# Performance work log

Hardware: AMD Instinct MI355X
Metric: run time of the kernel (lower is better)

Reference implementation:

```python
import jax, jax.numpy as jnp
import numpy as np

N_USERS = 100000
N_ITEMS = 50000
N_NODES = N_USERS + N_ITEMS
N_EDGES = 4800000
EMB_DIM = 64
N_LAYERS = 3


def setup_inputs() -> dict:
    key = jax.random.key(0)
    k1, k2, k3, k4, k5 = jax.random.split(key, 5)
    user_emb = jax.random.normal(k1, (N_USERS, EMB_DIM), dtype=jnp.float32)
    item_emb = jax.random.normal(k2, (N_ITEMS, EMB_DIM), dtype=jnp.float32)
    # COO representation of the (symmetric-normalized) adjacency matrix
    edge_src = jax.random.randint(k3, (N_EDGES,), 0, N_NODES, dtype=jnp.int32)
    edge_dst = jax.random.randint(k4, (N_EDGES,), 0, N_NODES, dtype=jnp.int32)
    edge_weight = jax.random.uniform(k5, (N_EDGES,), dtype=jnp.float32)
    return {
        "user_emb": user_emb,
        "item_emb": item_emb,
        "edge_weight": edge_weight,
        "edge_src": edge_src,
        "edge_dst": edge_dst,
    }


def _spmm(edge_src, edge_dst, edge_weight, x):
    # out[i] = sum_j A[i, j] * x[j]  with A in COO (dst=row i, src=col j)
    msgs = edge_weight[:, None] * x[edge_src]  # [E, D]
    return jax.ops.segment_sum(msgs, edge_dst, num_segments=N_NODES)


def reference(user_emb, item_emb, edge_weight, edge_src, edge_dst):
    ego = jnp.concatenate([user_emb, item_emb], axis=0)  # [N, D]
    acc = ego  # running sum over layer embeddings (layer 0 included)
    for _ in range(N_LAYERS):
        ego = _spmm(edge_src, edge_dst, edge_weight, ego)
        acc = acc + ego
    mean_emb = acc / jnp.float32(N_LAYERS + 1)  # mean over (L+1) layers
    new_user = mean_emb[:N_USERS]
    new_item = mean_emb[N_USERS:]
    return new_user, new_item
```

## Files before the change

### kernel.cpp

```cpp
#include <hip/hip_runtime.h>
#include <hip/hip_fp16.h>

#define N_USERS 100000
#define N_ITEMS 50000
#define N_NODES 150000
#define N_EDGES 4800000
#define EMB 64
#define N_LAYERS 3

#define NBKT 256
#define NPB  586
#define NREP 8
#define SUBCAP 2624
#define CAP (NREP * SUBCAP)

typedef unsigned int u32;
typedef unsigned short u16;
typedef u32 vu4 __attribute__((ext_vector_type(4)));
typedef u32 vu2 __attribute__((ext_vector_type(2)));
typedef float vf4 __attribute__((ext_vector_type(4)));

#define W_BITS 14
#define W_SCALE 16384.0f
#define W_INV   (1.0f / 16384.0f)
#define W_MASK  16383u

__device__ __forceinline__ float2 h2f(u32 v) {
    float2 r;
    r.x = __half2float(__ushort_as_half((u16)(v & 0xffffu)));
    r.y = __half2float(__ushort_as_half((u16)(v >> 16)));
    return r;
}

__global__ void k_init(const float4* __restrict__ user,
                       const float4* __restrict__ item,
                       ushort4* __restrict__ cur,
                       int* __restrict__ cursor) {
    int i = blockIdx.x * blockDim.x + threadIdx.x;
    const int total4 = N_NODES * EMB / 4;
    const int user4  = N_USERS * EMB / 4;
    if (i < NREP * NBKT) cursor[i] = 0;
    if (i >= total4) return;
    float4 v = (i < user4) ? user[i] : item[i - user4];
    ushort4 h;
    h.x = __half_as_ushort(__float2half_rn(v.x));
    h.y = __half_as_ushort(__float2half_rn(v.y));
    h.z = __half_as_ushort(__float2half_rn(v.z));
    h.w = __half_as_ushort(__float2half_rn(v.w));
    cur[i] = h;
}

__global__ __launch_bounds__(256) void k_p1(const int4*   __restrict__ src4,
                                            const int4*   __restrict__ dst4,
                                            const float4* __restrict__ w4,
                                            int* __restrict__ cursor,
                                            u32* __restrict__ pk_arr,
                                            u16* __restrict__ ld_arr) {
    __shared__ int hist[NBKT];
    __shared__ int base[NBKT];
    int tid = threadIdx.x;
    hist[tid] = 0;
    __syncthreads();

    int g0 = blockIdx.x * 512 + tid * 2;
    bool act = (g0 < N_EDGES / 4);

    u32 pk[8];
    u32 meta[8];
    if (act) {
        int4 d0 = dst4[g0], d1 = dst4[g0 + 1];
        int4 s0 = src4[g0], s1 = src4[g0 + 1];
        float4 f0 = w4[g0], f1 = w4[g0 + 1];
        int   ds[8] = {d0.x, d0.y, d0.z, d0.w, d1.x, d1.y, d1.z, d1.w};
        int   ss[8] = {s0.x, s0.y, s0.z, s0.w, s1.x, s1.y, s1.z, s1.w};
        float wf[8] = {f0.x, f0.y, f0.z, f0.w, f1.x, f1.y, f1.z, f1.w};
        #pragma unroll
        for (int k = 0; k < 8; ++k) {
            u32 d  = (u32)ds[k];
            u32 b  = d / NPB;
            u32 ld = d - b * NPB;
            int r  = atomicAdd(&hist[b], 1);
            u32 wq = (u32)(wf[k] * W_SCALE + 0.5f);
            if (wq > W_MASK) wq = W_MASK;
            pk[k]   = ((u32)ss[k] << W_BITS) | wq;
            meta[k] = ((u32)r << 18) | (b << 10) | ld;
        }
    }
    __syncthreads();

    int rep = blockIdx.x & (NREP - 1);
    int h = hist[tid];
    if (h > 0) base[tid] = atomicAdd(&cursor[rep * NBKT + tid], h);
    __syncthreads();

    if (act) {
        #pragma unroll
        for (int k = 0; k < 8; ++k) {
            u32 b  = (meta[k] >> 10) & 255u;
            u32 r  = meta[k] >> 18;
            u32 ld = meta[k] & 1023u;
            int pos = base[b] + (int)r;
            if (pos < SUBCAP) {
                size_t slot = (size_t)b * CAP + (size_t)rep * SUBCAP + pos;
                pk_arr[slot] = pk[k];
                ld_arr[slot] = (u16)ld;
            }
        }
    }
}

__global__ __launch_bounds__(1024) void k_p2(const int* __restrict__ cursor,
                                             const u32* __restrict__ pk_arr,
                                             const u16* __restrict__ ld_arr,
                                             int* __restrict__ row_ptr,
                                             u32* __restrict__ pairs) {
    __shared__ int hist[1024];
    __shared__ int cur[NPB];
    __shared__ int btot[NBKT];
    __shared__ int bsum[NBKT];
    int b = blockIdx.x;
    int tid = threadIdx.x;
    hist[tid] = 0;
    if (tid < NBKT) {
        int s = 0;
        #pragma unroll
        for (int r = 0; r < NREP; ++r) s += cursor[r * NBKT + tid];
        btot[tid] = s;
        bsum[tid] = s;
    }
    if (b == 0 && tid == 0) row_ptr[N_NODES] = N_EDGES;
    __syncthreads();
    for (int off = 1; off < NBKT; off <<= 1) {
        int t = 0;
        if (tid < NBKT && tid >= off) t = bsum[tid - off];
        __syncthreads();
        if (tid < NBKT && tid >= off) bsum[tid] += t;
        __syncthreads();
    }
    int gbase = bsum[b] - btot[b];

    int lo = b * NPB;
    int nb = N_NODES - lo; if (nb > NPB) nb = NPB;

    int n[NREP];
    #pragma unroll
    for (int r = 0; r < NREP; ++r) {
        int c = cursor[r * NBKT + b];
        n[r] = (c > SUBCAP) ? SUBCAP : c;
    }

    for (int r = 0; r < NREP; ++r) {
        const u16* p = ld_arr + (size_t)b * CAP + (size_t)r * SUBCAP;
        for (int i = tid; i < n[r]; i += 1024)
            atomicAdd(&hist[p[i]], 1);
    }
    __syncthreads();

    int val = hist[tid];
    for (int off = 1; off < 1024; off <<= 1) {
        int t = 0;
        if (tid >= off) t = hist[tid - off];
        __syncthreads();
        if (tid >= off) hist[tid] += t;
        __syncthreads();
    }
    int excl = hist[tid] - val;
    if (tid < nb) {
        row_ptr[lo + tid] = gbase + excl;
        cur[tid] = excl;
    }
    __syncthreads();

    for (int r = 0; r < NREP; ++r) {
        const u16* p = ld_arr + (size_t)b * CAP + (size_t)r * SUBCAP;
        const u32* q = pk_arr + (size_t)b * CAP + (size_t)r * SUBCAP;
        for (int i = tid; i < n[r]; i += 1024) {
            int ld  = p[i];
            int pos = atomicAdd(&cur[ld], 1);
            pairs[gbase + pos] = q[i];
        }
    }
}

struct Dec4 { u32 r0, r1, r2, r3; float w0, w1, w2, w3; };

__device__ __forceinline__ Dec4 dec_fast(vu4 p) {
    Dec4 d;
    d.r0 = p.x >> W_BITS; d.w0 = (float)(p.x & W_MASK) * W_INV;
    d.r1 = p.y >> W_BITS; d.w1 = (float)(p.y & W_MASK) * W_INV;
    d.r2 = p.z >> W_BITS; d.w2 = (float)(p.z & W_MASK) * W_INV;
    d.r3 = p.w >> W_BITS; d.w3 = (float)(p.w & W_MASK) * W_INV;
    return d;
}

__device__ __forceinline__ Dec4 dec_mask(vu4 p, int eb, int beg, int end) {
    Dec4 d;
    bool v0 = (eb + 0 >= beg) && (eb + 0 < end);
    bool v1 = (eb + 1 >= beg) && (eb + 1 < end);
    bool v2 = (eb + 2 >= beg) && (eb + 2 < end);
    bool v3 = (eb + 3 >= beg) && (eb + 3 < end);
    d.r0 = v0 ? (p.x >> W_BITS) : 0u; d.w0 = v0 ? (float)(p.x & W_MASK) * W_INV : 0.f;
    d.r1 = v1 ? (p.y >> W_BITS) : 0u; d.w1 = v1 ? (float)(p.y & W_MASK) * W_INV : 0.f;
    d.r2 = v2 ? (p.z >> W_BITS) : 0u; d.w2 = v2 ? (float)(p.z & W_MASK) * W_INV : 0.f;
    d.r3 = v3 ? (p.w >> W_BITS) : 0u; d.w3 = v3 ? (float)(p.w & W_MASK) * W_INV : 0.f;
    return d;
}

__device__ __forceinline__ Dec4 dec(vu4 p, int lo, int beg, int end, int g) {
    if (lo >= beg && lo + 16 <= end) return dec_fast(p);
    return dec_mask(p, lo + 4 * g, beg, end);
}

__device__ __forceinline__ vu2 ldx(const char* xbase, u32 r, u32 moff) {
    return *(const vu2*)(xbase + (size_t)(r * 128u + moff));
}

__device__ __forceinline__ void fmix2(float& a0, float& a1, float w, u32 x) {
    asm("v_fma_mix_f32 %0, %1, %2, %0 op_sel:[0,0,0] op_sel_hi:[0,1,0]"
        : "+v"(a0) : "v"(w), "v"(x));
    asm("v_fma_mix_f32 %0, %1, %2, %0 op_sel:[0,1,0] op_sel_hi:[0,1,0]"
        : "+v"(a1) : "v"(w), "v"(x));
}

__device__ __forceinline__ void acc4(vu2 xv, float w,
                                     float& ax, float& ay, float& az, float& aw) {
    fmix2(ax, ay, w, xv.x);
    fmix2(az, aw, w, xv.y);
}

#define LOADX(pfx, d) \
    vu2 pfx##0 = ldx(xbase, d.r0, moff), pfx##1 = ldx(xbase, d.r1, moff), \
        pfx##2 = ldx(xbase, d.r2, moff), pfx##3 = ldx(xbase, d.r3, moff)
#define ACCX(pfx, d) \
    acc4(pfx##0, d.w0, ax, ay, az, aw); acc4(pfx##1, d.w1, ax, ay, az, aw); \
    acc4(pfx##2, d.w2, ax, ay, az, aw); acc4(pfx##3, d.w3, ax, ay, az, aw)

template<int FIN>
__global__ __launch_bounds__(256) void k_gather(const int* __restrict__ row_ptr,
                                                const u32* __restrict__ pairs,
                                                const __half* __restrict__ x,
                                                __half* __restrict__ nxt,
                                                const float4* __restrict__ user,
                                                const float4* __restrict__ item,
                                                const ushort4* __restrict__ e1,
                                                const ushort4* __restrict__ e2,
                                                float* __restrict__ outp) {
    int wave = (blockIdx.x * blockDim.x + threadIdx.x) >> 6;
    int lane = threadIdx.x & 63;
    if (wave >= N_NODES) return;

    const int m = lane & 15;
    float4 ego = {};
    ushort4 pa = {}, pb = {};
    if (FIN && lane < 16) {
        size_t idx = (size_t)wave * 16 + m;
        const size_t user4 = (size_t)N_USERS * 16;
        ego = (idx < user4) ? user[idx] : item[idx - user4];
        pa = e1[idx];
        pb = e2[idx];
    }

    int beg = row_ptr[wave];
    int end = row_ptr[wave + 1];

    const int g = lane >> 4;
    const u32 moff = (u32)m << 3;
    const char* xbase = (const char*)x;

    float ax = 0.f, ay = 0.f, az = 0.f, aw = 0.f;

    int jb = beg & ~3;
    int nb = (end - jb + 15) >> 4;
    const u32* pp = pairs + jb + 4 * g;

    if (nb == 1) {
        vu4 P0 = __builtin_nontemporal_load((const vu4*)pp);
        Dec4 d0 = dec(P0, jb, beg, end, g);
        LOADX(xa, d0);
        ACCX(xa, d0);
    } else if (nb == 2) {
        vu4 P0 = __builtin_nontemporal_load((const vu4*)pp);
        vu4 P1 = __builtin_nontemporal_load((const vu4*)(pp + 16));
        Dec4 d0 = dec(P0, jb, beg, end, g);
        LOADX(xa, d0);
        Dec4 d1 = dec(P1, jb + 16, beg, end, g);
        LOADX(xc, d1);
        ACCX(xa, d0);
        ACCX(xc, d1);
    } else if (nb == 3) {
        vu4 P0 = __builtin_nontemporal_load((const vu4*)pp);
        vu4 P1 = __builtin_nontemporal_load((const vu4*)(pp + 16));
        vu4 P2 = __builtin_nontemporal_load((const vu4*)(pp + 32));
        Dec4 d0 = dec(P0, jb, beg, end, g);
        LOADX(xa, d0);
        Dec4 d1 = dec(P1, jb + 16, beg, end, g);
        LOADX(xc, d1);
        ACCX(xa, d0);
        Dec4 d2 = dec(P2, jb + 32, beg, end, g);
        LOADX(xd, d2);
        ACCX(xc, d1);
        ACCX(xd, d2);
    } else if (nb >= 4) {
        vu4 P0 = __builtin_nontemporal_load((const vu4*)pp);
        vu4 P1 = __builtin_nontemporal_load((const vu4*)(pp + 16));
        vu4 P2 = __builtin_nontemporal_load((const vu4*)(pp + 32));
        Dec4 d0 = dec(P0, jb, beg, end, g);
        LOADX(xa, d0);
        Dec4 d1 = dec(P1, jb + 16, beg, end, g);
        LOADX(xc, d1);
        ACCX(xa, d0);
        vu4 P3 = __builtin_nontemporal_load((const vu4*)(pp + 48));
        Dec4 d2 = dec(P2, jb + 32, beg, end, g);
        LOADX(xd, d2);
        ACCX(xc, d1);
        Dec4 d3 = dec(P3, jb + 48, beg, end, g);
        LOADX(xe, d3);
        ACCX(xd, d2);
        ACCX(xe, d3);
        for (int b = 4; b < nb; ++b) {
            vu4 Pl = __builtin_nontemporal_load((const vu4*)(pp + (size_t)16 * b));
            Dec4 dl = dec(Pl, jb + 16 * b, beg, end, g);
            LOADX(xf, dl);
            ACCX(xf, dl);
        }
    }

    ax += __shfl_xor(ax, 16); ax += __shfl_xor(ax, 32);
    ay += __shfl_xor(ay, 16); ay += __shfl_xor(ay, 32);
    az += __shfl_xor(az, 16); az += __shfl_xor(az, 32);
    aw += __shfl_xor(aw, 16); aw += __shfl_xor(aw, 32);

    if (lane < 16) {
        if (FIN) {
            vf4 o;
            o.x = (ego.x + __half2float(__ushort_as_half(pa.x))
                         + __half2float(__ushort_as_half(pb.x)) + ax) * 0.25f;
            o.y = (ego.y + __half2float(__ushort_as_half(pa.y))
                         + __half2float(__ushort_as_half(pb.y)) + ay) * 0.25f;
            o.z = (ego.z + __half2float(__ushort_as_half(pa.z))
                         + __half2float(__ushort_as_half(pb.z)) + az) * 0.25f;
            o.w = (ego.w + __half2float(__ushort_as_half(pa.w))
                         + __half2float(__ushort_as_half(pb.w)) + aw) * 0.25f;
            __builtin_nontemporal_store(o, (vf4*)outp + (size_t)wave * 16 + m);
        } else {
            ushort4 h;
            h.x = __half_as_ushort(__float2half_rn(ax));
            h.y = __half_as_ushort(__float2half_rn(ay));
            h.z = __half_as_ushort(__float2half_rn(az));
            h.w = __half_as_ushort(__float2half_rn(aw));
            ((ushort4*)nxt)[(size_t)wave * 16 + m] = h;
        }
    }
}

__global__ void k_spmm(const int*   __restrict__ src,
                       const int*   __restrict__ dst,
                       const float* __restrict__ w,
                       const float* __restrict__ x,
                       float*       __restrict__ y) {
    long long t = (long long)blockIdx.x * blockDim.x + threadIdx.x;
    int e = (int)(t >> 4);
    if (e >= N_EDGES) return;
    int q = (int)(t & 15);
    int   s  = src[e];
    int   d  = dst[e];
    float we = w[e];
    const float4* xs = (const float4*)(x + (long long)s * EMB);
    float4 v = xs[q];
    float* yd = y + (long long)d * EMB + q * 4;
    atomicAdd(yd + 0, we * v.x);
    atomicAdd(yd + 1, we * v.y);
    atomicAdd(yd + 2, we * v.z);
    atomicAdd(yd + 3, we * v.w);
}

__global__ void k_init_f32(const float4* __restrict__ user,
                           const float4* __restrict__ item,
                           float4* __restrict__ out,
                           float4* __restrict__ cur) {
    int i = blockIdx.x * blockDim.x + threadIdx.x;
    const int total4 = N_NODES * EMB / 4;
    const int user4  = N_USERS * EMB / 4;
    if (i >= total4) return;
    float4 v = (i < user4) ? user[i] : item[i - user4];
    out[i] = v;
    cur[i] = v;
}

__global__ void k_acc(float4* __restrict__ out,
                      const float4* __restrict__ buf,
                      float scale) {
    int i = blockIdx.x * blockDim.x + threadIdx.x;
    const int total4 = N_NODES * EMB / 4;
    if (i >= total4) return;
    float4 o = out[i];
    float4 b = buf[i];
    o.x = (o.x + b.x) * scale;
    o.y = (o.y + b.y) * scale;
    o.z = (o.z + b.z) * scale;
    o.w = (o.w + b.w) * scale;
    out[i] = o;
}

extern "C" void kernel_launch(void* const* d_in, const int* in_sizes, int n_in,
                              void* d_out, int out_size, void* d_ws, size_t ws_size,
                              hipStream_t stream) {
    const float* user_emb = (const float*)d_in[0];
    const float* item_emb = (const float*)d_in[1];
    const float* edge_w   = (const float*)d_in[2];
    const int*   edge_src = (const int*)d_in[3];
    const int*   edge_dst = (const int*)d_in[4];
    float* out = (float*)d_out;

    const size_t feat_elems = (size_t)N_NODES * EMB;
    const size_t feat_bytes_f32 = feat_elems * 4;
    const size_t feat_bytes_f16 = feat_elems * 2;

    char* ws = (char*)d_ws;
    size_t off = 0;
    __half* h0 = (__half*)(ws + off); off += feat_bytes_f16;
    __half* h1 = (__half*)(ws + off); off += feat_bytes_f16;
    __half* h2 = (__half*)(ws + off); off += feat_bytes_f16;
    int* row_ptr  = (int*)(ws + off); off += ((size_t)(N_NODES + 1) * 4 + 63) / 64 * 64;
    int* cursor   = (int*)(ws + off); off += (size_t)NREP * NBKT * 4;
    u32* pk_arr = (u32*)(ws + off);   off += (size_t)NBKT * CAP * 4;
    u16* ld_arr = (u16*)(ws + off);   off += (size_t)NBKT * CAP * 2;
    u32* pairs  = (u32*)(ws + off);   off += (size_t)N_EDGES * 4 + 64;
    const size_t needed = off;

    const int block = 256;
    const int total4 = (int)(feat_elems / 4);
    const int fgrid = (total4 + block - 1) / block;
    const int p1grid = (N_EDGES / 8 + block - 1) / block;
    const int ggrid = (N_NODES + 3) / 4;

    if (ws_size >= needed) {
        k_init<<<fgrid, block, 0, stream>>>((const float4*)user_emb,
                                            (const float4*)item_emb,
                                            (ushort4*)h0, cursor);

        k_p1<<<p1grid, block, 0, stream>>>((const int4*)edge_src,
                                           (const int4*)edge_dst,
                                           (const float4*)edge_w,
                                           cursor, pk_arr, ld_arr);
        k_p2<<<NBKT, 1024, 0, stream>>>(cursor, pk_arr, ld_arr,
                                        row_ptr, pairs);

        k_gather<0><<<ggrid, block, 0, stream>>>(row_ptr, pairs, h0, h1,
                                                 nullptr, nullptr, nullptr,
                                                 nullptr, nullptr);
        k_gather<0><<<ggrid, block, 0, stream>>>(row_ptr, pairs, h1, h2,
                                                 nullptr, nullptr, nullptr,
                                                 nullptr, nullptr);
        k_gather<1><<<ggrid, block, 0, stream>>>(row_ptr, pairs, h2, nullptr,
                                                 (const float4*)user_emb,
                                                 (const float4*)item_emb,
                                                 (const ushort4*)h1,
                                                 (const ushort4*)h2,
                                                 out);
    } else {
        float* buf0 = (float*)d_ws;
        float* buf1 = buf0 + feat_elems;
        k_init_f32<<<fgrid, block, 0, stream>>>((const float4*)user_emb,
                                                (const float4*)item_emb,
                                                (float4*)out, (float4*)buf0);
        float* cur = buf0;
        float* nxt = buf1;
        for (int layer = 0; layer < N_LAYERS; ++layer) {
            (void)hipMemsetAsync(nxt, 0, feat_bytes_f32, stream);
            long long threads = (long long)N_EDGES * 16;
            int grid = (int)((threads + block - 1) / block);
            k_spmm<<<grid, block, 0, stream>>>(edge_src, edge_dst, edge_w, cur, nxt);
            float scale = (layer == N_LAYERS - 1) ? (1.0f / (N_LAYERS + 1)) : 1.0f;
            k_acc<<<fgrid, block, 0, stream>>>((float4*)out, (const float4*)nxt, scale);
            float* tmp = cur; cur = nxt; nxt = tmp;
        }
    }
}
```

Measured before the change: 465.2 us.

## Process two rows per wave with interleaved gathers and deferred weight scaling

Each wave now handles two adjacent destination rows. It issues the first three pair blocks of both rows up front and interleaves their decode, gather and accumulate steps, so more independent memory loads are in flight per wave. The per-edge weight multiply by the fixed-point scale is dropped and applied once to the accumulator at the end. The final layer now reads the layer-0 embeddings from the fp16 copy instead of the fp32 inputs, which cuts bytes read but slightly lowers precision. Register pressure rises and the launch has half as many waves, which may reduce occupancy or worsen load balance between rows of different degree.

```diff
diff --git a/kernel.cpp b/kernel.cpp
--- a/kernel.cpp
+++ b/kernel.cpp
@@ -25,11 +25,8 @@
 #define W_INV   (1.0f / 16384.0f)
 #define W_MASK  16383u
 
-__device__ __forceinline__ float2 h2f(u32 v) {
-    float2 r;
-    r.x = __half2float(__ushort_as_half((u16)(v & 0xffffu)));
-    r.y = __half2float(__ushort_as_half((u16)(v >> 16)));
-    return r;
+__device__ __forceinline__ float hh(u16 v) {
+    return __half2float(__ushort_as_half(v));
 }
 
 __global__ void k_init(const float4* __restrict__ user,
@@ -186,10 +183,10 @@
 
 __device__ __forceinline__ Dec4 dec_fast(vu4 p) {
     Dec4 d;
-    d.r0 = p.x >> W_BITS; d.w0 = (float)(p.x & W_MASK) * W_INV;
-    d.r1 = p.y >> W_BITS; d.w1 = (float)(p.y & W_MASK) * W_INV;
-    d.r2 = p.z >> W_BITS; d.w2 = (float)(p.z & W_MASK) * W_INV;
-    d.r3 = p.w >> W_BITS; d.w3 = (float)(p.w & W_MASK) * W_INV;
+    d.r0 = p.x >> W_BITS; d.w0 = (float)(p.x & W_MASK);
+    d.r1 = p.y >> W_BITS; d.w1 = (float)(p.y & W_MASK);
+    d.r2 = p.z >> W_BITS; d.w2 = (float)(p.z & W_MASK);
+    d.r3 = p.w >> W_BITS; d.w3 = (float)(p.w & W_MASK);
     return d;
 }
 
@@ -199,16 +196,20 @@
     bool v1 = (eb + 1 >= beg) && (eb + 1 < end);
     bool v2 = (eb + 2 >= beg) && (eb + 2 < end);
     bool v3 = (eb + 3 >= beg) && (eb + 3 < end);
-    d.r0 = v0 ? (p.x >> W_BITS) : 0u; d.w0 = v0 ? (float)(p.x & W_MASK) * W_INV : 0.f;
-    d.r1 = v1 ? (p.y >> W_BITS) : 0u; d.w1 = v1 ? (float)(p.y & W_MASK) * W_INV : 0.f;
-    d.r2 = v2 ? (p.z >> W_BITS) : 0u; d.w2 = v2 ? (float)(p.z & W_MASK) * W_INV : 0.f;
-    d.r3 = v3 ? (p.w >> W_BITS) : 0u; d.w3 = v3 ? (float)(p.w & W_MASK) * W_INV : 0.f;
+    d.r0 = v0 ? (p.x >> W_BITS) : 0u; d.w0 = v0 ? (float)(p.x & W_MASK) : 0.f;
+    d.r1 = v1 ? (p.y >> W_BITS) : 0u; d.w1 = v1 ? (float)(p.y & W_MASK) : 0.f;
+    d.r2 = v2 ? (p.z >> W_BITS) : 0u; d.w2 = v2 ? (float)(p.z & W_MASK) : 0.f;
+    d.r3 = v3 ? (p.w >> W_BITS) : 0u; d.w3 = v3 ? (float)(p.w & W_MASK) : 0.f;
     return d;
 }
 
 __device__ __forceinline__ Dec4 dec(vu4 p, int lo, int beg, int end, int g) {
     if (lo >= beg && lo + 16 <= end) return dec_fast(p);
     return dec_mask(p, lo + 4 * g, beg, end);
+}
+
+__device__ __forceinline__ vu4 ldp(const u32* p) {
+    return __builtin_nontemporal_load((const vu4*)p);
 }
 
 __device__ __forceinline__ vu2 ldx(const char* xbase, u32 r, u32 moff) {
@@ -228,127 +229,119 @@
     fmix2(az, aw, w, xv.y);
 }
 
-#define LOADX(pfx, d) \
-    vu2 pfx##0 = ldx(xbase, d.r0, moff), pfx##1 = ldx(xbase, d.r1, moff), \
-        pfx##2 = ldx(xbase, d.r2, moff), pfx##3 = ldx(xbase, d.r3, moff)
-#define ACCX(pfx, d) \
-    acc4(pfx##0, d.w0, ax, ay, az, aw); acc4(pfx##1, d.w1, ax, ay, az, aw); \
-    acc4(pfx##2, d.w2, ax, ay, az, aw); acc4(pfx##3, d.w3, ax, ay, az, aw)
+#define DECLX(p) vu2 p##0 = {}, p##1 = {}, p##2 = {}, p##3 = {}
+#define LOADX2(p, d) \
+    p##0 = ldx(xbase, d.r0, moff); p##1 = ldx(xbase, d.r1, moff); \
+    p##2 = ldx(xbase, d.r2, moff); p##3 = ldx(xbase, d.r3, moff)
+#define ACC2(p, d, AX, AY, AZ, AW) \
+    acc4(p##0, d.w0, AX, AY, AZ, AW); acc4(p##1, d.w1, AX, AY, AZ, AW); \
+    acc4(p##2, d.w2, AX, AY, AZ, AW); acc4(p##3, d.w3, AX, AY, AZ, AW)
+#define RED(v) v += __shfl_xor(v, 16); v += __shfl_xor(v, 32)
 
 template<int FIN>
 __global__ __launch_bounds__(256) void k_gather(const int* __restrict__ row_ptr,
                                                 const u32* __restrict__ pairs,
                                                 const __half* __restrict__ x,
                                                 __half* __restrict__ nxt,
-                                                const float4* __restrict__ user,
-                                                const float4* __restrict__ item,
+                                                const ushort4* __restrict__ e0,
                                                 const ushort4* __restrict__ e1,
                                                 const ushort4* __restrict__ e2,
                                                 float* __restrict__ outp) {
-    int wave = (blockIdx.x * blockDim.x + threadIdx.x) >> 6;
+    int widx = (blockIdx.x * blockDim.x + threadIdx.x) >> 6;
     int lane = threadIdx.x & 63;
-    if (wave >= N_NODES) return;
+    if (widx >= N_NODES / 2) return;
+    const int rA = widx << 1;
 
     const int m = lane & 15;
-    float4 ego = {};
-    ushort4 pa = {}, pb = {};
-    if (FIN && lane < 16) {
-        size_t idx = (size_t)wave * 16 + m;
-        const size_t user4 = (size_t)N_USERS * 16;
-        ego = (idx < user4) ? user[idx] : item[idx - user4];
-        pa = e1[idx];
-        pb = e2[idx];
-    }
-
-    int beg = row_ptr[wave];
-    int end = row_ptr[wave + 1];
-
     const int g = lane >> 4;
     const u32 moff = (u32)m << 3;
     const char* xbase = (const char*)x;
 
-    float ax = 0.f, ay = 0.f, az = 0.f, aw = 0.f;
-
-    int jb = beg & ~3;
-    int nb = (end - jb + 15) >> 4;
-    const u32* pp = pairs + jb + 4 * g;
-
-    if (nb == 1) {
-        vu4 P0 = __builtin_nontemporal_load((const vu4*)pp);
-        Dec4 d0 = dec(P0, jb, beg, end, g);
-        LOADX(xa, d0);
-        ACCX(xa, d0);
-    } else if (nb == 2) {
-        vu4 P0 = __builtin_nontemporal_load((const vu4*)pp);
-        vu4 P1 = __builtin_nontemporal_load((const vu4*)(pp + 16));
-        Dec4 d0 = dec(P0, jb, beg, end, g);
-        LOADX(xa, d0);
-        Dec4 d1 = dec(P1, jb + 16, beg, end, g);
-        LOADX(xc, d1);
-        ACCX(xa, d0);
-        ACCX(xc, d1);
-    } else if (nb == 3) {
-        vu4 P0 = __builtin_nontemporal_load((const vu4*)pp);
-        vu4 P1 = __builtin_nontemporal_load((const vu4*)(pp + 16));
-        vu4 P2 = __builtin_nontemporal_load((const vu4*)(pp + 32));
-        Dec4 d0 = dec(P0, jb, beg, end, g);
-        LOADX(xa, d0);
-        Dec4 d1 = dec(P1, jb + 16, beg, end, g);
-        LOADX(xc, d1);
-        ACCX(xa, d0);
-        Dec4 d2 = dec(P2, jb + 32, beg, end, g);
-        LOADX(xd, d2);
-        ACCX(xc, d1);
-        ACCX(xd, d2);
-    } else if (nb >= 4) {
-        vu4 P0 = __builtin_nontemporal_load((const vu4*)pp);
-        vu4 P1 = __builtin_nontemporal_load((const vu4*)(pp + 16));
-        vu4 P2 = __builtin_nontemporal_load((const vu4*)(pp + 32));
-        Dec4 d0 = dec(P0, jb, beg, end, g);
-        LOADX(xa, d0);
-        Dec4 d1 = dec(P1, jb + 16, beg, end, g);
-        LOADX(xc, d1);
-        ACCX(xa, d0);
-        vu4 P3 = __builtin_nontemporal_load((const vu4*)(pp + 48));
-        Dec4 d2 = dec(P2, jb + 32, beg, end, g);
-        LOADX(xd, d2);
-        ACCX(xc, d1);
-        Dec4 d3 = dec(P3, jb + 48, beg, end, g);
-        LOADX(xe, d3);
-        ACCX(xd, d2);
-        ACCX(xe, d3);
-        for (int b = 4; b < nb; ++b) {
-            vu4 Pl = __builtin_nontemporal_load((const vu4*)(pp + (size_t)16 * b));
-            Dec4 dl = dec(Pl, jb + 16 * b, beg, end, g);
-            LOADX(xf, dl);
-            ACCX(xf, dl);
-        }
-    }
-
-    ax += __shfl_xor(ax, 16); ax += __shfl_xor(ax, 32);
-    ay += __shfl_xor(ay, 16); ay += __shfl_xor(ay, 32);
-    az += __shfl_xor(az, 16); az += __shfl_xor(az, 32);
-    aw += __shfl_xor(aw, 16); aw += __shfl_xor(aw, 32);
+    int a    = row_ptr[rA];
+    int bmid = row_ptr[rA + 1];
+    int cend = row_ptr[rA + 2];
+    int jbA = a & ~3, jbB = bmid & ~3;
+    int na = (bmid - jbA + 15) >> 4;
+    int nb = (cend - jbB + 15) >> 4;
+    const u32* ppA = pairs + jbA + 4 * g;
+    const u32* ppB = pairs + jbB + 4 * g;
+
+    float axA = 0.f, ayA = 0.f, azA = 0.f, awA = 0.f;
+    float axB = 0.f, ayB = 0.f, azB = 0.f, awB = 0.f;
+
+    vu4 PA0 = {}, PA1 = {}, PA2 = {}, PB0 = {}, PB1 = {}, PB2 = {};
+    if (na > 0) PA0 = ldp(ppA);
+    if (nb > 0) PB0 = ldp(ppB);
+    if (na > 1) PA1 = ldp(ppA + 16);
+    if (nb > 1) PB1 = ldp(ppB + 16);
+    if (na > 2) PA2 = ldp(ppA + 32);
+    if (nb > 2) PB2 = ldp(ppB + 32);
+
+    Dec4 dA0, dA1, dA2, dB0, dB1, dB2;
+    DECLX(xA0); DECLX(xA1); DECLX(xA2);
+    DECLX(xB0); DECLX(xB1); DECLX(xB2);
+
+    if (na > 0) { dA0 = dec(PA0, jbA,      a,    bmid, g); LOADX2(xA0, dA0); }
+    if (nb > 0) { dB0 = dec(PB0, jbB,      bmid, cend, g); LOADX2(xB0, dB0); }
+    if (na > 1) { dA1 = dec(PA1, jbA + 16, a,    bmid, g); LOADX2(xA1, dA1); }
+    if (na > 0) { ACC2(xA0, dA0, axA, ayA, azA, awA); }
+    if (nb > 1) { dB1 = dec(PB1, jbB + 16, bmid, cend, g); LOADX2(xB1, dB1); }
+    if (nb > 0) { ACC2(xB0, dB0, axB, ayB, azB, awB); }
+    if (na > 2) { dA2 = dec(PA2, jbA + 32, a,    bmid, g); LOADX2(xA2, dA2); }
+    if (na > 1) { ACC2(xA1, dA1, axA, ayA, azA, awA); }
+    if (nb > 2) { dB2 = dec(PB2, jbB + 32, bmid, cend, g); LOADX2(xB2, dB2); }
+    if (nb > 1) { ACC2(xB1, dB1, axB, ayB, azB, awB); }
+    if (na > 2) { ACC2(xA2, dA2, axA, ayA, azA, awA); }
+    if (nb > 2) { ACC2(xB2, dB2, axB, ayB, azB, awB); }
+
+    for (int t = 3; t < na; ++t) {
+        vu4 P = ldp(ppA + (size_t)16 * t);
+        Dec4 d = dec(P, jbA + 16 * t, a, bmid, g);
+        DECLX(xt); LOADX2(xt, d);
+        ACC2(xt, d, axA, ayA, azA, awA);
+    }
+    for (int t = 3; t < nb; ++t) {
+        vu4 P = ldp(ppB + (size_t)16 * t);
+        Dec4 d = dec(P, jbB + 16 * t, bmid, cend, g);
+        DECLX(xt); LOADX2(xt, d);
+        ACC2(xt, d, axB, ayB, azB, awB);
+    }
+
+    ushort4 ega = {}, eaa = {}, eba = {}, egb = {}, eab = {}, ebb = {};
+    if (FIN && lane < 16) {
+        size_t ia = (size_t)rA * 16 + m;
+        ega = e0[ia];      eaa = e1[ia];      eba = e2[ia];
+        egb = e0[ia + 16]; eab = e1[ia + 16]; ebb = e2[ia + 16];
+    }
+
+    RED(axA); RED(ayA); RED(azA); RED(awA);
+    RED(axB); RED(ayB); RED(azB); RED(awB);
 
     if (lane < 16) {
         if (FIN) {
-            vf4 o;
-            o.x = (ego.x + __half2float(__ushort_as_half(pa.x))
-                         + __half2float(__ushort_as_half(pb.x)) + ax) * 0.25f;
-            o.y = (ego.y + __half2float(__ushort_as_half(pa.y))
-                         + __half2float(__ushort_as_half(pb.y)) + ay) * 0.25f;
-            o.z = (ego.z + __half2float(__ushort_as_half(pa.z))
-                         + __half2float(__ushort_as_half(pb.z)) + az) * 0.25f;
-            o.w = (ego.w + __half2float(__ushort_as_half(pa.w))
-                         + __half2float(__ushort_as_half(pb.w)) + aw) * 0.25f;
-            __builtin_nontemporal_store(o, (vf4*)outp + (size_t)wave * 16 + m);
+            vf4 oA, oB;
+            oA.x = (hh(ega.x) + hh(eaa.x) + hh(eba.x) + axA * W_INV) * 0.25f;
+            oA.y = (hh(ega.y) + hh(eaa.y) + hh(eba.y) + ayA * W_INV) * 0.25f;
+            oA.z = (hh(ega.z) + hh(eaa.z) + hh(eba.z) + azA * W_INV) * 0.25f;
+            oA.w = (hh(ega.w) + hh(eaa.w) + hh(eba.w) + awA * W_INV) * 0.25f;
+            oB.x = (hh(egb.x) + hh(eab.x) + hh(ebb.x) + axB * W_INV) * 0.25f;
+            oB.y = (hh(egb.y) + hh(eab.y) + hh(ebb.y) + ayB * W_INV) * 0.25f;
+            oB.z = (hh(egb.z) + hh(eab.z) + hh(ebb.z) + azB * W_INV) * 0.25f;
+            oB.w = (hh(egb.w) + hh(eab.w) + hh(ebb.w) + awB * W_INV) * 0.25f;
+            __builtin_nontemporal_store(oA, (vf4*)outp + (size_t)rA * 16 + m);
+            __builtin_nontemporal_store(oB, (vf4*)outp + (size_t)rA * 16 + 16 + m);
         } else {
-            ushort4 h;
-            h.x = __half_as_ushort(__float2half_rn(ax));
-            h.y = __half_as_ushort(__float2half_rn(ay));
-            h.z = __half_as_ushort(__float2half_rn(az));
-            h.w = __half_as_ushort(__float2half_rn(aw));
-            ((ushort4*)nxt)[(size_t)wave * 16 + m] = h;
+            ushort4 hA, hB;
+            hA.x = __half_as_ushort(__float2half_rn(axA * W_INV));
+            hA.y = __half_as_ushort(__float2half_rn(ayA * W_INV));
+            hA.z = __half_as_ushort(__float2half_rn(azA * W_INV));
+            hA.w = __half_as_ushort(__float2half_rn(awA * W_INV));
+            hB.x = __half_as_ushort(__float2half_rn(axB * W_INV));
+            hB.y = __half_as_ushort(__float2half_rn(ayB * W_INV));
+            hB.z = __half_as_ushort(__float2half_rn(azB * W_INV));
+            hB.w = __half_as_ushort(__float2half_rn(awB * W_INV));
+            ((ushort4*)nxt)[(size_t)rA * 16 + m] = hA;
+            ((ushort4*)nxt)[(size_t)rA * 16 + 16 + m] = hB;
         }
     }
 }
@@ -432,7 +425,7 @@
     const int total4 = (int)(feat_elems / 4);
     const int fgrid = (total4 + block - 1) / block;
     const int p1grid = (N_EDGES / 8 + block - 1) / block;
-    const int ggrid = (N_NODES + 3) / 4;
+    const int ggrid = (N_NODES / 2 + 3) / 4;
 
     if (ws_size >= needed) {
         k_init<<<fgrid, block, 0, stream>>>((const float4*)user_emb,
@@ -448,13 +441,12 @@
 
         k_gather<0><<<ggrid, block, 0, stream>>>(row_ptr, pairs, h0, h1,
                                                  nullptr, nullptr, nullptr,
-                                                 nullptr, nullptr);
+                                                 nullptr);
         k_gather<0><<<ggrid, block, 0, stream>>>(row_ptr, pairs, h1, h2,
                                                  nullptr, nullptr, nullptr,
-                                                 nullptr, nullptr);
+                                                 nullptr);
         k_gather<1><<<ggrid, block, 0, stream>>>(row_ptr, pairs, h2, nullptr,
-                                                 (const float4*)user_emb,
-                                                 (const float4*)item_emb,
+                                                 (const ushort4*)h0,
                                                  (const ushort4*)h1,
                                                  (const ushort4*)h2,
                                                  out);
```

New measurement: 471.9 us. Within noise of the previous version (+1.4%).

## Stage bucket scatter through LDS, defer weight scaling, read fp16 layer-0 in final pass

Applied to the files above, without the earlier changes.

The edge bucketing kernel now sorts its 2048 edges by bucket in shared memory with a block-wide prefix scan, then writes them out in bucket order so global stores are contiguous runs rather than scattered. The gather kernels drop the per-edge multiply by the weight dequant scale and apply it once after the reduction. The final layer reads the fp16 copy of the input embeddings instead of the fp32 user/item arrays, halving that read but using fp16-rounded layer-0 values in the mean. The prefix scan adds several block barriers to the bucketing kernel.

```diff
diff --git a/kernel.cpp b/kernel.cpp
--- a/kernel.cpp
+++ b/kernel.cpp
@@ -25,11 +25,8 @@
 #define W_INV   (1.0f / 16384.0f)
 #define W_MASK  16383u
 
-__device__ __forceinline__ float2 h2f(u32 v) {
-    float2 r;
-    r.x = __half2float(__ushort_as_half((u16)(v & 0xffffu)));
-    r.y = __half2float(__ushort_as_half((u16)(v >> 16)));
-    return r;
+__device__ __forceinline__ float hh(u16 v) {
+    return __half2float(__ushort_as_half(v));
 }
 
 __global__ void k_init(const float4* __restrict__ user,
@@ -58,6 +55,9 @@
                                             u16* __restrict__ ld_arr) {
     __shared__ int hist[NBKT];
     __shared__ int base[NBKT];
+    __shared__ int bscan[NBKT];
+    __shared__ u32 s_pk[2048];
+    __shared__ u32 s_meta[2048];
     int tid = threadIdx.x;
     hist[tid] = 0;
     __syncthreads();
@@ -67,6 +67,7 @@
 
     u32 pk[8];
     u32 meta[8];
+    int rk[8];
     if (act) {
         int4 d0 = dst4[g0], d1 = dst4[g0 + 1];
         int4 s0 = src4[g0], s1 = src4[g0 + 1];
@@ -79,11 +80,11 @@
             u32 d  = (u32)ds[k];
             u32 b  = d / NPB;
             u32 ld = d - b * NPB;
-            int r  = atomicAdd(&hist[b], 1);
+            rk[k]  = atomicAdd(&hist[b], 1);
             u32 wq = (u32)(wf[k] * W_SCALE + 0.5f);
             if (wq > W_MASK) wq = W_MASK;
             pk[k]   = ((u32)ss[k] << W_BITS) | wq;
-            meta[k] = ((u32)r << 18) | (b << 10) | ld;
+            meta[k] = (b << 10) | ld;
         }
     }
     __syncthreads();
@@ -91,19 +92,39 @@
     int rep = blockIdx.x & (NREP - 1);
     int h = hist[tid];
     if (h > 0) base[tid] = atomicAdd(&cursor[rep * NBKT + tid], h);
-    __syncthreads();
+    bscan[tid] = h;
+    __syncthreads();
+    for (int off = 1; off < NBKT; off <<= 1) {
+        int t = 0;
+        if (tid >= off) t = bscan[tid - off];
+        __syncthreads();
+        if (tid >= off) bscan[tid] += t;
+        __syncthreads();
+    }
 
     if (act) {
         #pragma unroll
         for (int k = 0; k < 8; ++k) {
-            u32 b  = (meta[k] >> 10) & 255u;
-            u32 r  = meta[k] >> 18;
-            u32 ld = meta[k] & 1023u;
-            int pos = base[b] + (int)r;
+            u32 b = meta[k] >> 10;
+            int s = (bscan[b] - hist[b]) + rk[k];
+            s_pk[s]   = pk[k];
+            s_meta[s] = meta[k];
+        }
+    }
+    __syncthreads();
+
+    int total = bscan[NBKT - 1];
+    #pragma unroll
+    for (int k = 0; k < 8; ++k) {
+        int s = k * 256 + tid;
+        if (s < total) {
+            u32 mt = s_meta[s];
+            u32 b  = mt >> 10;
+            int pos = base[b] + (s - (bscan[b] - hist[b]));
             if (pos < SUBCAP) {
                 size_t slot = (size_t)b * CAP + (size_t)rep * SUBCAP + pos;
-                pk_arr[slot] = pk[k];
-                ld_arr[slot] = (u16)ld;
+                pk_arr[slot] = s_pk[s];
+                ld_arr[slot] = (u16)(mt & 1023u);
             }
         }
     }
@@ -186,10 +207,10 @@
 
 __device__ __forceinline__ Dec4 dec_fast(vu4 p) {
     Dec4 d;
-    d.r0 = p.x >> W_BITS; d.w0 = (float)(p.x & W_MASK) * W_INV;
-    d.r1 = p.y >> W_BITS; d.w1 = (float)(p.y & W_MASK) * W_INV;
-    d.r2 = p.z >> W_BITS; d.w2 = (float)(p.z & W_MASK) * W_INV;
-    d.r3 = p.w >> W_BITS; d.w3 = (float)(p.w & W_MASK) * W_INV;
+    d.r0 = p.x >> W_BITS; d.w0 = (float)(p.x & W_MASK);
+    d.r1 = p.y >> W_BITS; d.w1 = (float)(p.y & W_MASK);
+    d.r2 = p.z >> W_BITS; d.w2 = (float)(p.z & W_MASK);
+    d.r3 = p.w >> W_BITS; d.w3 = (float)(p.w & W_MASK);
     return d;
 }
 
@@ -199,16 +220,20 @@
     bool v1 = (eb + 1 >= beg) && (eb + 1 < end);
     bool v2 = (eb + 2 >= beg) && (eb + 2 < end);
     bool v3 = (eb + 3 >= beg) && (eb + 3 < end);
-    d.r0 = v0 ? (p.x >> W_BITS) : 0u; d.w0 = v0 ? (float)(p.x & W_MASK) * W_INV : 0.f;
-    d.r1 = v1 ? (p.y >> W_BITS) : 0u; d.w1 = v1 ? (float)(p.y & W_MASK) * W_INV : 0.f;
-    d.r2 = v2 ? (p.z >> W_BITS) : 0u; d.w2 = v2 ? (float)(p.z & W_MASK) * W_INV : 0.f;
-    d.r3 = v3 ? (p.w >> W_BITS) : 0u; d.w3 = v3 ? (float)(p.w & W_MASK) * W_INV : 0.f;
+    d.r0 = v0 ? (p.x >> W_BITS) : 0u; d.w0 = v0 ? (float)(p.x & W_MASK) : 0.f;
+    d.r1 = v1 ? (p.y >> W_BITS) : 0u; d.w1 = v1 ? (float)(p.y & W_MASK) : 0.f;
+    d.r2 = v2 ? (p.z >> W_BITS) : 0u; d.w2 = v2 ? (float)(p.z & W_MASK) : 0.f;
+    d.r3 = v3 ? (p.w >> W_BITS) : 0u; d.w3 = v3 ? (float)(p.w & W_MASK) : 0.f;
     return d;
 }
 
 __device__ __forceinline__ Dec4 dec(vu4 p, int lo, int beg, int end, int g) {
     if (lo >= beg && lo + 16 <= end) return dec_fast(p);
     return dec_mask(p, lo + 4 * g, beg, end);
+}
+
+__device__ __forceinline__ vu4 ldp(const u32* p) {
+    return __builtin_nontemporal_load((const vu4*)p);
 }
 
 __device__ __forceinline__ vu2 ldx(const char* xbase, u32 r, u32 moff) {
@@ -234,14 +259,14 @@
 #define ACCX(pfx, d) \
     acc4(pfx##0, d.w0, ax, ay, az, aw); acc4(pfx##1, d.w1, ax, ay, az, aw); \
     acc4(pfx##2, d.w2, ax, ay, az, aw); acc4(pfx##3, d.w3, ax, ay, az, aw)
+#define RED(v) v += __shfl_xor(v, 16); v += __shfl_xor(v, 32)
 
 template<int FIN>
 __global__ __launch_bounds__(256) void k_gather(const int* __restrict__ row_ptr,
                                                 const u32* __restrict__ pairs,
                                                 const __half* __restrict__ x,
                                                 __half* __restrict__ nxt,
-                                                const float4* __restrict__ user,
-                                                const float4* __restrict__ item,
+                                                const ushort4* __restrict__ e0,
                                                 const ushort4* __restrict__ e1,
                                                 const ushort4* __restrict__ e2,
                                                 float* __restrict__ outp) {
@@ -250,14 +275,10 @@
     if (wave >= N_NODES) return;
 
     const int m = lane & 15;
-    float4 ego = {};
-    ushort4 pa = {}, pb = {};
+    ushort4 ega = {}, ea = {}, eb = {};
     if (FIN && lane < 16) {
         size_t idx = (size_t)wave * 16 + m;
-        const size_t user4 = (size_t)N_USERS * 16;
-        ego = (idx < user4) ? user[idx] : item[idx - user4];
-        pa = e1[idx];
-        pb = e2[idx];
+        ega = e0[idx]; ea = e1[idx]; eb = e2[idx];
     }
 
     int beg = row_ptr[wave];
@@ -274,13 +295,13 @@
     const u32* pp = pairs + jb + 4 * g;
 
     if (nb == 1) {
-        vu4 P0 = __builtin_nontemporal_load((const vu4*)pp);
+        vu4 P0 = ldp(pp);
         Dec4 d0 = dec(P0, jb, beg, end, g);
         LOADX(xa, d0);
         ACCX(xa, d0);
     } else if (nb == 2) {
-        vu4 P0 = __builtin_nontemporal_load((const vu4*)pp);
-        vu4 P1 = __builtin_nontemporal_load((const vu4*)(pp + 16));
+        vu4 P0 = ldp(pp);
+        vu4 P1 = ldp(pp + 16);
         Dec4 d0 = dec(P0, jb, beg, end, g);
         LOADX(xa, d0);
         Dec4 d1 = dec(P1, jb + 16, beg, end, g);
@@ -288,9 +309,9 @@
         ACCX(xa, d0);
         ACCX(xc, d1);
     } else if (nb == 3) {
-        vu4 P0 = __builtin_nontemporal_load((const vu4*)pp);
-        vu4 P1 = __builtin_nontemporal_load((const vu4*)(pp + 16));
-        vu4 P2 = __builtin_nontemporal_load((const vu4*)(pp + 32));
+        vu4 P0 = ldp(pp);
+        vu4 P1 = ldp(pp + 16);
+        vu4 P2 = ldp(pp + 32);
         Dec4 d0 = dec(P0, jb, beg, end, g);
         LOADX(xa, d0);
         Dec4 d1 = dec(P1, jb + 16, beg, end, g);
@@ -301,15 +322,15 @@
         ACCX(xc, d1);
         ACCX(xd, d2);
     } else if (nb >= 4) {
-        vu4 P0 = __builtin_nontemporal_load((const vu4*)pp);
-        vu4 P1 = __builtin_nontemporal_load((const vu4*)(pp + 16));
-        vu4 P2 = __builtin_nontemporal_load((const vu4*)(pp + 32));
+        vu4 P0 = ldp(pp);
+        vu4 P1 = ldp(pp + 16);
+        vu4 P2 = ldp(pp + 32);
         Dec4 d0 = dec(P0, jb, beg, end, g);
         LOADX(xa, d0);
         Dec4 d1 = dec(P1, jb + 16, beg, end, g);
         LOADX(xc, d1);
         ACCX(xa, d0);
-        vu4 P3 = __builtin_nontemporal_load((const vu4*)(pp + 48));
+        vu4 P3 = ldp(pp + 48);
         Dec4 d2 = dec(P2, jb + 32, beg, end, g);
         LOADX(xd, d2);
         ACCX(xc, d1);
@@ -318,36 +339,29 @@
         ACCX(xd, d2);
         ACCX(xe, d3);
         for (int b = 4; b < nb; ++b) {
-            vu4 Pl = __builtin_nontemporal_load((const vu4*)(pp + (size_t)16 * b));
+            vu4 Pl = ldp(pp + (size_t)16 * b);
             Dec4 dl = dec(Pl, jb + 16 * b, beg, end, g);
             LOADX(xf, dl);
             ACCX(xf, dl);
         }
     }
 
-    ax += __shfl_xor(ax, 16); ax += __shfl_xor(ax, 32);
-    ay += __shfl_xor(ay, 16); ay += __shfl_xor(ay, 32);
-    az += __shfl_xor(az, 16); az += __shfl_xor(az, 32);
-    aw += __shfl_xor(aw, 16); aw += __shfl_xor(aw, 32);
+    RED(ax); RED(ay); RED(az); RED(aw);
 
     if (lane < 16) {
         if (FIN) {
             vf4 o;
-            o.x = (ego.x + __half2float(__ushort_as_half(pa.x))
-                         + __half2float(__ushort_as_half(pb.x)) + ax) * 0.25f;
-            o.y = (ego.y + __half2float(__ushort_as_half(pa.y))
-                         + __half2float(__ushort_as_half(pb.y)) + ay) * 0.25f;
-            o.z = (ego.z + __half2float(__ushort_as_half(pa.z))
-                         + __half2float(__ushort_as_half(pb.z)) + az) * 0.25f;
-            o.w = (ego.w + __half2float(__ushort_as_half(pa.w))
-                         + __half2float(__ushort_as_half(pb.w)) + aw) * 0.25f;
+            o.x = (hh(ega.x) + hh(ea.x) + hh(eb.x) + ax * W_INV) * 0.25f;
+            o.y = (hh(ega.y) + hh(ea.y) + hh(eb.y) + ay * W_INV) * 0.25f;
+            o.z = (hh(ega.z) + hh(ea.z) + hh(eb.z) + az * W_INV) * 0.25f;
+            o.w = (hh(ega.w) + hh(ea.w) + hh(eb.w) + aw * W_INV) * 0.25f;
             __builtin_nontemporal_store(o, (vf4*)outp + (size_t)wave * 16 + m);
         } else {
             ushort4 h;
-            h.x = __half_as_ushort(__float2half_rn(ax));
-            h.y = __half_as_ushort(__float2half_rn(ay));
-            h.z = __half_as_ushort(__float2half_rn(az));
-            h.w = __half_as_ushort(__float2half_rn(aw));
+            h.x = __half_as_ushort(__float2half_rn(ax * W_INV));
+            h.y = __half_as_ushort(__float2half_rn(ay * W_INV));
+            h.z = __half_as_ushort(__float2half_rn(az * W_INV));
+            h.w = __half_as_ushort(__float2half_rn(aw * W_INV));
             ((ushort4*)nxt)[(size_t)wave * 16 + m] = h;
         }
     }
@@ -448,13 +462,12 @@
 
         k_gather<0><<<ggrid, block, 0, stream>>>(row_ptr, pairs, h0, h1,
                                                  nullptr, nullptr, nullptr,
-                                                 nullptr, nullptr);
+                                                 nullptr);
         k_gather<0><<<ggrid, block, 0, stream>>>(row_ptr, pairs, h1, h2,
                                                  nullptr, nullptr, nullptr,
-                                                 nullptr, nullptr);
+                                                 nullptr);
         k_gather<1><<<ggrid, block, 0, stream>>>(row_ptr, pairs, h2, nullptr,
-                                                 (const float4*)user_emb,
-                                                 (const float4*)item_emb,
+                                                 (const ushort4*)h0,
                                                  (const ushort4*)h1,
                                                  (const ushort4*)h2,
                                                  out);
```

New measurement: 442.4 us. -4.9%, faster.
